# Kernel tuning notes

Hardware: AMD Instinct MI355X
Metric: run time of the kernel (lower is better)

## Reference

```python
import jax, jax.numpy as jnp
import numpy as np

L = 5          # num_layer
D = 128        # emb_dim
N = 150000     # nodes
E = 500000     # edges
NF_ATOM, VA = 9, 119   # OGB atom feature count / max vocab
NF_BOND, VB = 3, 6     # OGB bond feature count / max vocab
BN_EPS = 1e-5


def setup_inputs() -> dict:
    key = jax.random.key(0)
    ks = jax.random.split(key, 10)
    s = 0.1
    x = jax.random.randint(ks[0], (N, NF_ATOM), 0, VA)
    edge_index = jax.random.randint(ks[1], (2, E), 0, N)
    edge_attr = jax.random.randint(ks[2], (E, NF_BOND), 0, VB)
    batch = jnp.sort(jax.random.randint(ks[3], (N,), 0, 2000))
    atom_emb = s * jax.random.normal(ks[4], (NF_ATOM, VA, D), dtype=jnp.float32)
    bond_emb = s * jax.random.normal(ks[5], (L, NF_BOND, VB, D), dtype=jnp.float32)
    eps = jnp.zeros((L,), jnp.float32)
    W1 = s * jax.random.normal(ks[6], (L, D, 2 * D), dtype=jnp.float32)
    b1 = jnp.zeros((L, 2 * D), jnp.float32)
    bn1_g = jnp.ones((L, 2 * D), jnp.float32)
    bn1_b = jnp.zeros((L, 2 * D), jnp.float32)
    W2 = s * jax.random.normal(ks[7], (L, 2 * D, D), dtype=jnp.float32)
    b2 = jnp.zeros((L, D), jnp.float32)
    bn_g = jnp.ones((L, D), jnp.float32)
    bn_b = jnp.zeros((L, D), jnp.float32)
    return dict(x=x, edge_index=edge_index, edge_attr=edge_attr, batch=batch,
                atom_emb=atom_emb, bond_emb=bond_emb, eps=eps,
                W1=W1, b1=b1, bn1_g=bn1_g, bn1_b=bn1_b,
                W2=W2, b2=b2, bn_g=bn_g, bn_b=bn_b)


def _bn(z, g, b):
    # BatchNorm1d with batch statistics (training-mode normalization)
    m = jnp.mean(z, axis=0)
    v = jnp.var(z, axis=0)
    return (z - m) * jax.lax.rsqrt(v + BN_EPS) * g + b


def _sum_embed(tables, idx):
    # tables: [F, V, D], idx: [n, F] -> sum_f tables[f][idx[:, f]] -> [n, D]
    return jax.vmap(lambda t, i: t[i], in_axes=(0, 1))(tables, idx).sum(0)


def reference(x, edge_index, edge_attr, batch, atom_emb, bond_emb, eps,
              W1, b1, bn1_g, bn1_b, W2, b2, bn_g, bn_b):
    n = x.shape[0]
    src, dst = edge_index[0], edge_index[1]
    h = _sum_embed(atom_emb, x)                      # AtomEncoder: [N, D]
    for l in range(L):
        e = _sum_embed(bond_emb[l], edge_attr)       # BondEncoder: [E, D]
        msg = jax.nn.relu(h[src] + e)                # message: gather + add + ReLU
        aggr = jax.ops.segment_sum(msg, dst, num_segments=n)  # scatter-add
        z = (1.0 + eps[l]) * h + aggr
        z = z @ W1[l] + b1[l]                        # [N, 2D]
        z = jax.nn.relu(_bn(z, bn1_g[l], bn1_b[l]))
        z = z @ W2[l] + b2[l]                        # [N, D]
        z = _bn(z, bn_g[l], bn_b[l])                 # outer BatchNorm
        if l < L - 1:
            z = jax.nn.relu(z)
        # dropout is identity in eval mode
        h = z + h                                    # residual
    return h  # JK='last'
```

## Files before the change

kernel.cpp:

```cpp
#include <hip/hip_runtime.h>

#define N_NODES 150000
#define N_EDGES 500000
#define D 128
#define D2 256
#define NLAYER 5
#define NB1 586
#define NROWT 9375
#define NBLK1 512
#define NBLK2 512

typedef __attribute__((ext_vector_type(8))) short bf16x8;
typedef __attribute__((ext_vector_type(4))) float f32x4;
typedef __attribute__((ext_vector_type(4))) unsigned short ushort4v;
typedef __attribute__((ext_vector_type(8))) unsigned short ushort8v;
typedef __attribute__((ext_vector_type(4))) unsigned int u32x4;

__device__ __forceinline__ unsigned short f2bf(float f) {
    unsigned int u = __builtin_bit_cast(unsigned int, f);
    u += 0x7fffu + ((u >> 16) & 1u);
    return (unsigned short)(u >> 16);
}
__device__ __forceinline__ unsigned short f2bf_hw(float f) {
    return __builtin_bit_cast(unsigned short, (__bf16)f);
}
__device__ __forceinline__ float bf2f(unsigned short s) {
    unsigned int u = ((unsigned int)s) << 16;
    return __builtin_bit_cast(float, u);
}

__global__ __launch_bounds__(256) void prepw_kernel(const float* __restrict__ W1,
        const float* __restrict__ W2, unsigned short* __restrict__ w1t,
        unsigned short* __restrict__ w2t) {
    int i = blockIdx.x * 256 + threadIdx.x;
    if (i < NLAYER * D2 * D) {
        int l = i / (D2 * D);
        int rem = i % (D2 * D);
        int n = rem / D;
        int k = rem % D;
        w1t[i] = f2bf(W1[(l * D + k) * D2 + n]);
    }
    if (i < NLAYER * D * D2) {
        int l = i / (D * D2);
        int rem = i % (D * D2);
        int n = rem / D2;
        int k = rem % D2;
        w2t[i] = f2bf(W2[(l * D2 + k) * D + n]);
    }
}

__global__ __launch_bounds__(128) void combo_kernel(const float* __restrict__ bemb,
        float* __restrict__ combo) {
    int b = blockIdx.x;
    int l = b / 216, p = b % 216;
    int a0 = p % 6, a1 = (p / 6) % 6, a2 = p / 36;
    int d = threadIdx.x;
    combo[b * D + d] = bemb[((l * 3 + 0) * 6 + a0) * D + d]
                     + bemb[((l * 3 + 1) * 6 + a1) * D + d]
                     + bemb[((l * 3 + 2) * 6 + a2) * D + d];
}

__global__ __launch_bounds__(256) void atom_enc_kernel(const int* __restrict__ x,
        const float* __restrict__ aemb, unsigned short* __restrict__ hbf) {
    int node = blockIdx.x * 8 + (threadIdx.x >> 5);
    int t = threadIdx.x & 31;
    int d0 = t * 4;
    f32x4 s = {0, 0, 0, 0};
#pragma unroll
    for (int f = 0; f < 9; ++f) {
        int xi = x[node * 9 + f];
        f32x4 v = *(const f32x4*)(aemb + (size_t)(f * 119 + xi) * D + d0);
        s[0] += v[0]; s[1] += v[1]; s[2] += v[2]; s[3] += v[3];
    }
    ushort4v o;
#pragma unroll
    for (int j = 0; j < 4; ++j) o[j] = f2bf_hw(s[j]);
    *(ushort4v*)(hbf + (size_t)node * D + d0) = o;
}

__global__ __launch_bounds__(256) void hist_kernel(const int* __restrict__ ei,
        int* __restrict__ deg) {
    int e = blockIdx.x * 256 + threadIdx.x;
    if (e < N_EDGES) atomicAdd(&deg[ei[N_EDGES + e]], 1);
}

__global__ __launch_bounds__(256) void scan1_kernel(const int* __restrict__ deg,
        int* __restrict__ part, int* __restrict__ bsum) {
    __shared__ int sd[256];
    int tid = threadIdx.x;
    int i = blockIdx.x * 256 + tid;
    int v = (i < N_NODES) ? deg[i] : 0;
    sd[tid] = v;
    __syncthreads();
    for (int off = 1; off < 256; off <<= 1) {
        int t = (tid >= off) ? sd[tid - off] : 0;
        __syncthreads();
        sd[tid] += t;
        __syncthreads();
    }
    if (i < N_NODES) part[i] = sd[tid] - v;
    if (tid == 255) bsum[blockIdx.x] = sd[255];
}

__global__ __launch_bounds__(1024) void scan2_kernel(const int* __restrict__ bsum,
        int* __restrict__ boff) {
    __shared__ int sd[1024];
    int tid = threadIdx.x;
    int v = (tid < NB1) ? bsum[tid] : 0;
    sd[tid] = v;
    __syncthreads();
    for (int off = 1; off < 1024; off <<= 1) {
        int t = (tid >= off) ? sd[tid - off] : 0;
        __syncthreads();
        sd[tid] += t;
        __syncthreads();
    }
    if (tid < NB1) boff[tid] = sd[tid] - v;
}

__global__ __launch_bounds__(256) void scan3_kernel(const int* __restrict__ part,
        const int* __restrict__ boff, int* __restrict__ row_start) {
    int i = blockIdx.x * 256 + threadIdx.x;
    if (i < N_NODES) row_start[i] = part[i] + boff[i >> 8];
}

__global__ __launch_bounds__(256) void bin_kernel(const int* __restrict__ ei,
        const int* __restrict__ ea, const int* __restrict__ row_start,
        int* __restrict__ cursor, int* __restrict__ bins) {
    int e = blockIdx.x * 256 + threadIdx.x;
    if (e >= N_EDGES) return;
    int dst = ei[N_EDGES + e];
    int pos = row_start[dst] + atomicAdd(&cursor[dst], 1);
    int pack = ea[e * 3 + 0] + ea[e * 3 + 1] * 6 + ea[e * 3 + 2] * 36;
    bins[pos] = ei[e] | (pack << 18);
}

__global__ __launch_bounds__(256) void aggr_kernel(const int* __restrict__ row_start,
        const int* __restrict__ deg, const int* __restrict__ bins,
        const float* __restrict__ combo, const unsigned short* __restrict__ hbf,
        const float* __restrict__ epsp, unsigned short* __restrict__ A) {
    int wid = threadIdx.x >> 6;
    int lane = threadIdx.x & 63;
    int sub = lane >> 4;
    int t = lane & 15;
    int d0 = t * 8;
    int node = blockIdx.x * 16 + wid * 4 + sub;
    float ke = 1.0f + epsp[0];
    int start = row_start[node];
    int dg = deg[node];
    f32x4 s0 = {0, 0, 0, 0}, s1 = {0, 0, 0, 0};
    int entry = (dg > 0) ? bins[start] : 0;
    for (int i = 0; i < dg; ++i) {
        int next = (i + 1 < dg) ? bins[start + i + 1] : 0;
        int src = entry & 0x3FFFF;
        int pack = entry >> 18;
        ushort8v hv = *(const ushort8v*)(hbf + (size_t)src * D + d0);
        f32x4 c0 = *(const f32x4*)(combo + pack * D + d0);
        f32x4 c1 = *(const f32x4*)(combo + pack * D + d0 + 4);
#pragma unroll
        for (int j = 0; j < 4; ++j) {
            s0[j] += fmaxf(bf2f(hv[j]) + c0[j], 0.f);
            s1[j] += fmaxf(bf2f(hv[j + 4]) + c1[j], 0.f);
        }
        entry = next;
    }
    ushort8v hs = *(const ushort8v*)(hbf + (size_t)node * D + d0);
    ushort8v o;
#pragma unroll
    for (int j = 0; j < 4; ++j) {
        o[j]     = f2bf_hw(ke * bf2f(hs[j]) + s0[j]);
        o[j + 4] = f2bf_hw(ke * bf2f(hs[j + 4]) + s1[j]);
    }
    *(ushort8v*)(A + (size_t)node * D + d0) = o;
}

__global__ __launch_bounds__(256) void gemm1s_kernel(const unsigned short* __restrict__ A,
        const unsigned short* __restrict__ w1t, const float* __restrict__ b1,
        float* __restrict__ part1) {
    int wave = threadIdx.x >> 6;
    int lane = threadIdx.x & 63;
    int l15 = lane & 15;
    int kg = lane >> 4;

    bf16x8 B[4][4];
    float bias[4];
#pragma unroll
    for (int t = 0; t < 4; ++t) {
        int col = (wave * 4 + t) * 16 + l15;
        bias[t] = b1[col];
#pragma unroll
        for (int kk = 0; kk < 4; ++kk)
            B[t][kk] = *(const bf16x8*)(w1t + (size_t)col * D + kk * 32 + kg * 8);
    }
    float s[4] = {0.f, 0.f, 0.f, 0.f}, q[4] = {0.f, 0.f, 0.f, 0.f};

    int rt = blockIdx.x;
    bf16x8 afn[4];
    {
        int row = rt * 16 + l15;
#pragma unroll
        for (int kk = 0; kk < 4; ++kk)
            afn[kk] = *(const bf16x8*)(A + (size_t)row * D + kk * 32 + kg * 8);
    }
    while (rt < NROWT) {
        int rtn = rt + NBLK1;
        bf16x8 af[4];
#pragma unroll
        for (int kk = 0; kk < 4; ++kk) af[kk] = afn[kk];
        if (rtn < NROWT) {
            int row = rtn * 16 + l15;
#pragma unroll
            for (int kk = 0; kk < 4; ++kk)
                afn[kk] = *(const bf16x8*)(A + (size_t)row * D + kk * 32 + kg * 8);
        }
        f32x4 acc[4];
#pragma unroll
        for (int t = 0; t < 4; ++t) acc[t] = (f32x4){0.f, 0.f, 0.f, 0.f};
#pragma unroll
        for (int kk = 0; kk < 4; ++kk)
#pragma unroll
            for (int t = 0; t < 4; ++t)
                acc[t] = __builtin_amdgcn_mfma_f32_16x16x32_bf16(af[kk], B[t][kk], acc[t], 0, 0, 0);
#pragma unroll
        for (int t = 0; t < 4; ++t) {
#pragma unroll
            for (int r = 0; r < 4; ++r) {
                float va = acc[t][r] + bias[t];
                s[t] += va;
                q[t] = fmaf(va, va, q[t]);
            }
        }
        rt = rtn;
    }
#pragma unroll
    for (int t = 0; t < 4; ++t) {
        s[t] += __shfl_xor(s[t], 16); s[t] += __shfl_xor(s[t], 32);
        q[t] += __shfl_xor(q[t], 16); q[t] += __shfl_xor(q[t], 32);
        if (kg == 0) {
            int col = (wave * 4 + t) * 16 + l15;
            part1[(size_t)blockIdx.x * 512 + col] = s[t];
            part1[(size_t)blockIdx.x * 512 + 256 + col] = q[t];
        }
    }
}

__global__ __launch_bounds__(256) void reduce_finalize_kernel(const float* __restrict__ part,
        int nblk, int C, const float* __restrict__ g, const float* __restrict__ bb,
        float* __restrict__ scale, float* __restrict__ shift,
        unsigned short* __restrict__ shpb) {
    int c = blockIdx.x;
    int tid = threadIdx.x;
    float s = 0.f, q = 0.f;
    for (int i = tid; i < nblk; i += 256) {
        s += part[(size_t)i * 2 * C + c];
        q += part[(size_t)i * 2 * C + C + c];
    }
#pragma unroll
    for (int off = 1; off < 64; off <<= 1) {
        s += __shfl_xor(s, off);
        q += __shfl_xor(q, off);
    }
    __shared__ float rs[4], rq[4];
    int w = tid >> 6;
    if ((tid & 63) == 0) { rs[w] = s; rq[w] = q; }
    __syncthreads();
    if (tid == 0) {
        s = rs[0] + rs[1] + rs[2] + rs[3];
        q = rq[0] + rq[1] + rq[2] + rq[3];
        float inv_n = 1.0f / (float)N_NODES;
        float mean = s * inv_n;
        float var = q * inv_n - mean * mean;
        float sc = g[c] * rsqrtf(var + 1e-5f);
        float sh = bb[c] - mean * sc;
        scale[c] = sc;
        shift[c] = sh;
        shpb[c] = f2bf(sh / sc);
    }
}

__global__ __launch_bounds__(256) void gemm12_kernel(const unsigned short* __restrict__ A,
        const unsigned short* __restrict__ w1t, const float* __restrict__ b1,
        const unsigned short* __restrict__ shpb, const float* __restrict__ scale1,
        const unsigned short* __restrict__ w2t, const float* __restrict__ b2,
        unsigned short* __restrict__ z2, float* __restrict__ part2) {
    __shared__ unsigned short z1t[16][264];
    __shared__ unsigned short sm2[4][16][44];
    int wave = threadIdx.x >> 6;
    int lane = threadIdx.x & 63;
    int l15 = lane & 15;
    int kg = lane >> 4;
    int rrow = lane >> 2;
    int rcol = (lane & 3) * 8;

    bf16x8 B1[4][4];
    float bs1[4];
#pragma unroll
    for (int t = 0; t < 4; ++t) {
        int col = (wave * 4 + t) * 16 + l15;
        bs1[t] = b1[col] + bf2f(shpb[col]);
#pragma unroll
        for (int kk = 0; kk < 4; ++kk)
            B1[t][kk] = *(const bf16x8*)(w1t + (size_t)col * D + kk * 32 + kg * 8);
    }
    bf16x8 B2[2][8];
    float bias2[2];
#pragma unroll
    for (int t = 0; t < 2; ++t) {
        int col = (wave * 2 + t) * 16 + l15;
        bias2[t] = b2[col];
#pragma unroll
        for (int kk = 0; kk < 8; ++kk) {
            bf16x8 raw = *(const bf16x8*)(w2t + (size_t)col * D2 + kk * 32 + kg * 8);
            int k0 = kk * 32 + kg * 8;
            const f32x4* sp = (const f32x4*)(scale1 + k0);
            f32x4 s0 = sp[0], s1 = sp[1];
            ushort8v bw;
#pragma unroll
            for (int j = 0; j < 4; ++j) {
                bw[j]     = f2bf_hw(bf2f((unsigned short)raw[j]) * s0[j]);
                bw[j + 4] = f2bf_hw(bf2f((unsigned short)raw[j + 4]) * s1[j]);
            }
            B2[t][kk] = __builtin_bit_cast(bf16x8, bw);
        }
    }

    float s[2] = {0.f, 0.f}, q[2] = {0.f, 0.f};

    int rt = blockIdx.x;
    bf16x8 afn[4];
    {
        int row = rt * 16 + l15;
#pragma unroll
        for (int kk = 0; kk < 4; ++kk)
            afn[kk] = *(const bf16x8*)(A + (size_t)row * D + kk * 32 + kg * 8);
    }
    while (rt < NROWT) {
        int rtn = rt + NBLK2;
        bf16x8 af[4];
#pragma unroll
        for (int kk = 0; kk < 4; ++kk) af[kk] = afn[kk];
        if (rtn < NROWT) {
            int row = rtn * 16 + l15;
#pragma unroll
            for (int kk = 0; kk < 4; ++kk)
                afn[kk] = *(const bf16x8*)(A + (size_t)row * D + kk * 32 + kg * 8);
        }
        f32x4 acc1[4];
#pragma unroll
        for (int t = 0; t < 4; ++t) acc1[t] = (f32x4){0.f, 0.f, 0.f, 0.f};
#pragma unroll
        for (int kk = 0; kk < 4; ++kk)
#pragma unroll
            for (int t = 0; t < 4; ++t)
                acc1[t] = __builtin_amdgcn_mfma_f32_16x16x32_bf16(af[kk], B1[t][kk], acc1[t], 0, 0, 0);
        __syncthreads();
#pragma unroll
        for (int t = 0; t < 4; ++t) {
            int col = (wave * 4 + t) * 16 + l15;
#pragma unroll
            for (int r = 0; r < 4; ++r)
                z1t[kg * 4 + r][col] = f2bf_hw(fmaxf(acc1[t][r] + bs1[t], 0.f));
        }
        __syncthreads();
        f32x4 acc2[2];
        acc2[0] = (f32x4){0.f, 0.f, 0.f, 0.f};
        acc2[1] = (f32x4){0.f, 0.f, 0.f, 0.f};
#pragma unroll
        for (int kk = 0; kk < 8; ++kk) {
            bf16x8 a2 = __builtin_bit_cast(bf16x8, *(const ushort8v*)&z1t[l15][kk * 32 + kg * 8]);
            acc2[0] = __builtin_amdgcn_mfma_f32_16x16x32_bf16(a2, B2[0][kk], acc2[0], 0, 0, 0);
            acc2[1] = __builtin_amdgcn_mfma_f32_16x16x32_bf16(a2, B2[1][kk], acc2[1], 0, 0, 0);
        }
#pragma unroll
        for (int t = 0; t < 2; ++t) {
#pragma unroll
            for (int r = 0; r < 4; ++r) {
                float va = acc2[t][r] + bias2[t];
                s[t] += va;
                q[t] = fmaf(va, va, q[t]);
                sm2[wave][kg * 4 + r][t * 16 + l15] = f2bf_hw(va);
            }
        }
        ushort8v v0 = *(const ushort8v*)&sm2[wave][rrow][rcol];
        *(ushort8v*)(z2 + (size_t)(rt * 16 + rrow) * D + wave * 32 + rcol) = v0;
        rt = rtn;
    }
#pragma unroll
    for (int t = 0; t < 2; ++t) {
        s[t] += __shfl_xor(s[t], 16); s[t] += __shfl_xor(s[t], 32);
        q[t] += __shfl_xor(q[t], 16); q[t] += __shfl_xor(q[t], 32);
        if (kg == 0) {
            int col = (wave * 2 + t) * 16 + l15;
            part2[(size_t)blockIdx.x * 256 + col] = s[t];
            part2[(size_t)blockIdx.x * 256 + 128 + col] = q[t];
        }
    }
}

__global__ __launch_bounds__(256) void final_kernel(const unsigned short* __restrict__ z2,
        const float* __restrict__ scale, const float* __restrict__ shift,
        unsigned short* __restrict__ hbf, float* __restrict__ hout, int last) {
    int i = blockIdx.x * 256 + threadIdx.x;
    int base = i * 8;
    int c = base & (D - 1);
    f32x4 sc0 = *(const f32x4*)(scale + c);
    f32x4 sc1 = *(const f32x4*)(scale + c + 4);
    f32x4 sh0 = *(const f32x4*)(shift + c);
    f32x4 sh1 = *(const f32x4*)(shift + c + 4);
    ushort8v zv = *(const ushort8v*)(z2 + base);
    ushort8v hv = *(const ushort8v*)(hbf + base);
    if (last) {
        f32x4 o0, o1;
#pragma unroll
        for (int j = 0; j < 4; ++j) {
            o0[j] = fmaf(bf2f(zv[j]), sc0[j], sh0[j]) + bf2f(hv[j]);
            o1[j] = fmaf(bf2f(zv[j + 4]), sc1[j], sh1[j]) + bf2f(hv[j + 4]);
        }
        *(f32x4*)(hout + base) = o0;
        *(f32x4*)(hout + base + 4) = o1;
    } else {
        ushort8v ob;
#pragma unroll
        for (int j = 0; j < 4; ++j) {
            float v0 = fmaxf(fmaf(bf2f(zv[j]), sc0[j], sh0[j]), 0.f) + bf2f(hv[j]);
            float v1 = fmaxf(fmaf(bf2f(zv[j + 4]), sc1[j], sh1[j]), 0.f) + bf2f(hv[j + 4]);
            ob[j] = f2bf_hw(v0);
            ob[j + 4] = f2bf_hw(v1);
        }
        *(ushort8v*)(hbf + base) = ob;
    }
}

extern "C" void kernel_launch(void* const* d_in, const int* in_sizes, int n_in,
                              void* d_out, int out_size, void* d_ws, size_t ws_size,
                              hipStream_t stream) {
    const int* x = (const int*)d_in[0];
    const int* ei = (const int*)d_in[1];
    const int* ea = (const int*)d_in[2];
    const float* aemb = (const float*)d_in[4];
    const float* bemb = (const float*)d_in[5];
    const float* eps = (const float*)d_in[6];
    const float* W1 = (const float*)d_in[7];
    const float* b1 = (const float*)d_in[8];
    const float* bn1g = (const float*)d_in[9];
    const float* bn1b = (const float*)d_in[10];
    const float* W2 = (const float*)d_in[11];
    const float* b2 = (const float*)d_in[12];
    const float* bng = (const float*)d_in[13];
    const float* bnb = (const float*)d_in[14];
    float* h = (float*)d_out;

    char* ws = (char*)d_ws;
    size_t off = 0;
    auto alloc = [&](size_t bytes) {
        void* p = ws + off;
        off += (bytes + 255) & ~(size_t)255;
        return p;
    };
    unsigned short* Az2 = (unsigned short*)alloc((size_t)N_NODES * D * 2);
    unsigned short* hbf = (unsigned short*)alloc((size_t)N_NODES * D * 2);
    unsigned short* w1t = (unsigned short*)alloc((size_t)NLAYER * D2 * D * 2);
    unsigned short* w2t = (unsigned short*)alloc((size_t)NLAYER * D * D2 * 2);
    float* combo        = (float*)alloc((size_t)NLAYER * 216 * D * 4);
    int* bins           = (int*)alloc((size_t)N_EDGES * 4);
    int* row_start      = (int*)alloc((size_t)(NB1 * 256) * 4);
    int* deg            = (int*)alloc((size_t)(NB1 * 256) * 4);
    int* cursor         = (int*)alloc((size_t)(NB1 * 256) * 4);
    int* part           = (int*)alloc((size_t)(NB1 * 256) * 4);
    int* bsum           = (int*)alloc(1024 * 4);
    int* boff           = (int*)alloc(1024 * 4);
    float* part1        = (float*)alloc((size_t)NBLK1 * 512 * 4);
    float* part2        = (float*)alloc((size_t)NBLK2 * 256 * 4);
    float* scale1 = (float*)alloc(256 * 4);
    float* shift1 = (float*)alloc(256 * 4);
    float* scale2 = (float*)alloc(128 * 4);
    float* shift2 = (float*)alloc(128 * 4);
    unsigned short* shp1 = (unsigned short*)alloc(256 * 2);
    unsigned short* shp2 = (unsigned short*)alloc(128 * 2);

    prepw_kernel<<<(NLAYER * D2 * D + 255) / 256, 256, 0, stream>>>(W1, W2, w1t, w2t);
    combo_kernel<<<NLAYER * 216, 128, 0, stream>>>(bemb, combo);
    atom_enc_kernel<<<N_NODES / 8, 256, 0, stream>>>(x, aemb, hbf);

    hipMemsetAsync(deg, 0, (size_t)(NB1 * 256) * 4, stream);
    hipMemsetAsync(cursor, 0, (size_t)(NB1 * 256) * 4, stream);
    hist_kernel<<<(N_EDGES + 255) / 256, 256, 0, stream>>>(ei, deg);
    scan1_kernel<<<NB1, 256, 0, stream>>>(deg, part, bsum);
    scan2_kernel<<<1, 1024, 0, stream>>>(bsum, boff);
    scan3_kernel<<<NB1, 256, 0, stream>>>(part, boff, row_start);
    bin_kernel<<<(N_EDGES + 255) / 256, 256, 0, stream>>>(ei, ea, row_start, cursor, bins);

    for (int l = 0; l < NLAYER; ++l) {
        aggr_kernel<<<N_NODES / 16, 256, 0, stream>>>(row_start, deg, bins,
                combo + l * 216 * D, hbf, eps + l, Az2);
        gemm1s_kernel<<<NBLK1, 256, 0, stream>>>(Az2, w1t + l * D2 * D,
                b1 + l * D2, part1);
        reduce_finalize_kernel<<<256, 256, 0, stream>>>(part1, NBLK1, D2,
                bn1g + l * D2, bn1b + l * D2, scale1, shift1, shp1);
        gemm12_kernel<<<NBLK2, 256, 0, stream>>>(Az2, w1t + l * D2 * D,
                b1 + l * D2, shp1, scale1, w2t + l * D * D2, b2 + l * D, Az2, part2);
        reduce_finalize_kernel<<<128, 256, 0, stream>>>(part2, NBLK2, D,
                bng + l * D, bnb + l * D, scale2, shift2, shp2);
        final_kernel<<<(N_NODES * D / 8) / 256, 256, 0, stream>>>(Az2, scale2, shift2,
                hbf, h, (l == NLAYER - 1) ? 1 : 0);
    }
}
```

Baseline: 714.7 us.

## Fuse first-GEMM batch-norm statistics into the aggregation kernel

The aggregation kernel now stages each block's 16 aggregated rows in shared memory and runs the first MFMA GEMM on them directly. It accumulates per-column sum and sum-of-squares into 512 slots with float atomics, which removes the separate gemm1s pass that re-read the aggregated matrix. In exchange, each of the 9375 blocks must load the full W1 tile into registers, which raises register pressure and may lower occupancy in the gather-bound aggregation. It also adds atomic contention and a memset per layer.

Result: slower. 1.102 ms (+54.2%).

```diff
diff --git a/kernel.cpp b/kernel.cpp
--- a/kernel.cpp
+++ b/kernel.cpp
@@ -7,8 +7,8 @@
 #define NLAYER 5
 #define NB1 586
 #define NROWT 9375
-#define NBLK1 512
 #define NBLK2 512
+#define NP1 512
 
 typedef __attribute__((ext_vector_type(8))) short bf16x8;
 typedef __attribute__((ext_vector_type(4))) float f32x4;
@@ -138,13 +138,31 @@
 __global__ __launch_bounds__(256) void aggr_kernel(const int* __restrict__ row_start,
         const int* __restrict__ deg, const int* __restrict__ bins,
         const float* __restrict__ combo, const unsigned short* __restrict__ hbf,
-        const float* __restrict__ epsp, unsigned short* __restrict__ A) {
+        const float* __restrict__ epsp, const unsigned short* __restrict__ w1t,
+        const float* __restrict__ b1, unsigned short* __restrict__ A,
+        float* __restrict__ part1) {
+    __shared__ unsigned short at[16][136];
     int wid = threadIdx.x >> 6;
     int lane = threadIdx.x & 63;
     int sub = lane >> 4;
     int t = lane & 15;
     int d0 = t * 8;
-    int node = blockIdx.x * 16 + wid * 4 + sub;
+    int row = wid * 4 + sub;
+    int node = blockIdx.x * 16 + row;
+    int l15 = lane & 15;
+    int kg = lane >> 4;
+
+    bf16x8 B[4][4];
+    float bias[4];
+#pragma unroll
+    for (int tt = 0; tt < 4; ++tt) {
+        int col = (wid * 4 + tt) * 16 + l15;
+        bias[tt] = b1[col];
+#pragma unroll
+        for (int kk = 0; kk < 4; ++kk)
+            B[tt][kk] = *(const bf16x8*)(w1t + (size_t)col * D + kk * 32 + kg * 8);
+    }
+
     float ke = 1.0f + epsp[0];
     int start = row_start[node];
     int dg = deg[node];
@@ -172,74 +190,35 @@
         o[j + 4] = f2bf_hw(ke * bf2f(hs[j + 4]) + s1[j]);
     }
     *(ushort8v*)(A + (size_t)node * D + d0) = o;
-}
-
-__global__ __launch_bounds__(256) void gemm1s_kernel(const unsigned short* __restrict__ A,
-        const unsigned short* __restrict__ w1t, const float* __restrict__ b1,
-        float* __restrict__ part1) {
-    int wave = threadIdx.x >> 6;
-    int lane = threadIdx.x & 63;
-    int l15 = lane & 15;
-    int kg = lane >> 4;
-
-    bf16x8 B[4][4];
-    float bias[4];
-#pragma unroll
-    for (int t = 0; t < 4; ++t) {
-        int col = (wave * 4 + t) * 16 + l15;
-        bias[t] = b1[col];
-#pragma unroll
-        for (int kk = 0; kk < 4; ++kk)
-            B[t][kk] = *(const bf16x8*)(w1t + (size_t)col * D + kk * 32 + kg * 8);
-    }
-    float s[4] = {0.f, 0.f, 0.f, 0.f}, q[4] = {0.f, 0.f, 0.f, 0.f};
-
-    int rt = blockIdx.x;
-    bf16x8 afn[4];
-    {
-        int row = rt * 16 + l15;
-#pragma unroll
-        for (int kk = 0; kk < 4; ++kk)
-            afn[kk] = *(const bf16x8*)(A + (size_t)row * D + kk * 32 + kg * 8);
-    }
-    while (rt < NROWT) {
-        int rtn = rt + NBLK1;
-        bf16x8 af[4];
-#pragma unroll
-        for (int kk = 0; kk < 4; ++kk) af[kk] = afn[kk];
-        if (rtn < NROWT) {
-            int row = rtn * 16 + l15;
-#pragma unroll
-            for (int kk = 0; kk < 4; ++kk)
-                afn[kk] = *(const bf16x8*)(A + (size_t)row * D + kk * 32 + kg * 8);
-        }
-        f32x4 acc[4];
-#pragma unroll
-        for (int t = 0; t < 4; ++t) acc[t] = (f32x4){0.f, 0.f, 0.f, 0.f};
-#pragma unroll
-        for (int kk = 0; kk < 4; ++kk)
-#pragma unroll
-            for (int t = 0; t < 4; ++t)
-                acc[t] = __builtin_amdgcn_mfma_f32_16x16x32_bf16(af[kk], B[t][kk], acc[t], 0, 0, 0);
-#pragma unroll
-        for (int t = 0; t < 4; ++t) {
-#pragma unroll
-            for (int r = 0; r < 4; ++r) {
-                float va = acc[t][r] + bias[t];
-                s[t] += va;
-                q[t] = fmaf(va, va, q[t]);
-            }
-        }
-        rt = rtn;
-    }
-#pragma unroll
-    for (int t = 0; t < 4; ++t) {
-        s[t] += __shfl_xor(s[t], 16); s[t] += __shfl_xor(s[t], 32);
-        q[t] += __shfl_xor(q[t], 16); q[t] += __shfl_xor(q[t], 32);
+    *(ushort8v*)&at[row][d0] = o;
+    __syncthreads();
+
+    f32x4 acc[4];
+#pragma unroll
+    for (int tt = 0; tt < 4; ++tt) acc[tt] = (f32x4){0.f, 0.f, 0.f, 0.f};
+#pragma unroll
+    for (int kk = 0; kk < 4; ++kk) {
+        bf16x8 af = __builtin_bit_cast(bf16x8, *(const ushort8v*)&at[l15][kk * 32 + kg * 8]);
+#pragma unroll
+        for (int tt = 0; tt < 4; ++tt)
+            acc[tt] = __builtin_amdgcn_mfma_f32_16x16x32_bf16(af, B[tt][kk], acc[tt], 0, 0, 0);
+    }
+#pragma unroll
+    for (int tt = 0; tt < 4; ++tt) {
+        float s = 0.f, q = 0.f;
+#pragma unroll
+        for (int r = 0; r < 4; ++r) {
+            float va = acc[tt][r] + bias[tt];
+            s += va;
+            q = fmaf(va, va, q);
+        }
+        s += __shfl_xor(s, 16); s += __shfl_xor(s, 32);
+        q += __shfl_xor(q, 16); q += __shfl_xor(q, 32);
         if (kg == 0) {
-            int col = (wave * 4 + t) * 16 + l15;
-            part1[(size_t)blockIdx.x * 512 + col] = s[t];
-            part1[(size_t)blockIdx.x * 512 + 256 + col] = q[t];
+            int col = (wid * 4 + tt) * 16 + l15;
+            int slot = blockIdx.x & (NP1 - 1);
+            atomicAdd(&part1[(size_t)slot * 512 + col], s);
+            atomicAdd(&part1[(size_t)slot * 512 + 256 + col], q);
         }
     }
 }
@@ -469,7 +448,7 @@
     int* part           = (int*)alloc((size_t)(NB1 * 256) * 4);
     int* bsum           = (int*)alloc(1024 * 4);
     int* boff           = (int*)alloc(1024 * 4);
-    float* part1        = (float*)alloc((size_t)NBLK1 * 512 * 4);
+    float* part1        = (float*)alloc((size_t)NP1 * 512 * 4);
     float* part2        = (float*)alloc((size_t)NBLK2 * 256 * 4);
     float* scale1 = (float*)alloc(256 * 4);
     float* shift1 = (float*)alloc(256 * 4);
@@ -491,11 +470,11 @@
     bin_kernel<<<(N_EDGES + 255) / 256, 256, 0, stream>>>(ei, ea, row_start, cursor, bins);
 
     for (int l = 0; l < NLAYER; ++l) {
+        hipMemsetAsync(part1, 0, (size_t)NP1 * 512 * 4, stream);
         aggr_kernel<<<N_NODES / 16, 256, 0, stream>>>(row_start, deg, bins,
-                combo + l * 216 * D, hbf, eps + l, Az2);
-        gemm1s_kernel<<<NBLK1, 256, 0, stream>>>(Az2, w1t + l * D2 * D,
-                b1 + l * D2, part1);
-        reduce_finalize_kernel<<<256, 256, 0, stream>>>(part1, NBLK1, D2,
+                combo + l * 216 * D, hbf, eps + l, w1t + l * D2 * D, b1 + l * D2,
+                Az2, part1);
+        reduce_finalize_kernel<<<256, 256, 0, stream>>>(part1, NP1, D2,
                 bn1g + l * D2, bn1b + l * D2, scale1, shift1, shp1);
         gemm12_kernel<<<NBLK2, 256, 0, stream>>>(Az2, w1t + l * D2 * D,
                 b1 + l * D2, shp1, scale1, w2t + l * D * D2, b2 + l * D, Az2, part2);
```
